# Performance work log

Hardware: AMD Instinct MI355X
Metric: run time of the kernel (lower is better)

Reference implementation:

```python
import jax, jax.numpy as jnp
import numpy as np

B, T = 256, 512          # sequences, timesteps (batched over pyro.markov loop)
DATA_DIM = 88            # piano-roll tones
HIDDEN_DIM = 16          # HMM latent states
NN_DIM = 48
NN_CHANNELS = 2
KERNEL = 3


def _uniform(key, shape, fan_in):
    bound = 1.0 / np.sqrt(fan_in)
    return jax.random.uniform(key, shape, minval=-bound, maxval=bound, dtype=jnp.float32)


def setup_inputs() -> dict:
    key = jax.random.key(0)
    ks = jax.random.split(key, 13)
    w = jax.random.randint(ks[0], (B, T, 1), 0, HIDDEN_DIM)
    x = jax.random.randint(ks[1], (B, T, 1), 0, HIDDEN_DIM)
    y = jax.random.uniform(ks[2], (B, T, DATA_DIM), dtype=jnp.float32)
    return {
        "w": w, "x": x, "y": y,
        # nn.Linear(hidden_dim, nn_dim) for x and w one-hots
        "W_xh": _uniform(ks[3], (NN_DIM, HIDDEN_DIM), HIDDEN_DIM),
        "b_xh": _uniform(ks[4], (NN_DIM,), HIDDEN_DIM),
        "W_wh": _uniform(ks[5], (NN_DIM, HIDDEN_DIM), HIDDEN_DIM),
        "b_wh": _uniform(ks[6], (NN_DIM,), HIDDEN_DIM),
        # nn.Linear(nn_channels*data_dim, nn_dim)
        "W_yh": _uniform(ks[7], (NN_DIM, NN_CHANNELS * DATA_DIM), NN_CHANNELS * DATA_DIM),
        "b_yh": _uniform(ks[8], (NN_DIM,), NN_CHANNELS * DATA_DIM),
        # nn.Conv1d(1, nn_channels, 3, padding=1)
        "W_conv": _uniform(ks[9], (NN_CHANNELS, 1, KERNEL), KERNEL),
        "b_conv": _uniform(ks[10], (NN_CHANNELS,), KERNEL),
        # nn.Linear(nn_dim, data_dim)
        "W_hl": _uniform(ks[11], (DATA_DIM, NN_DIM), NN_DIM),
        "b_hl": _uniform(ks[12], (DATA_DIM,), NN_DIM),
    }


def _tones_generator(w, x, y, W_xh, b_xh, W_wh, b_wh, W_yh, b_yh, W_conv, b_conv, W_hl, b_hl):
    b, t, d = y.shape
    # one-hot scatter of the latent state indices (trailing index dim of size 1)
    w_onehot = jax.nn.one_hot(w[..., 0], HIDDEN_DIM, dtype=y.dtype)   # [B,T,H]
    x_onehot = jax.nn.one_hot(x[..., 0], HIDDEN_DIM, dtype=y.dtype)   # [B,T,H]
    # Conv1d(1 -> nn_channels, k=3, pad=1) over the tone axis
    y_nch = y.reshape(b * t, 1, d)                                    # [BT,1,D]
    y_conv = jax.lax.conv_general_dilated(
        y_nch, W_conv, window_strides=(1,), padding=[(1, 1)],
        dimension_numbers=("NCH", "OIH", "NCH"))
    y_conv = jax.nn.relu(y_conv + b_conv[None, :, None])              # [BT,C,D]
    y_conv = y_conv.reshape(b, t, NN_CHANNELS * d)                    # [B,T,C*D]
    h = jax.nn.relu(
        jnp.einsum("bth,nh->btn", x_onehot, W_xh) + b_xh
        + jnp.einsum("bth,nh->btn", w_onehot, W_wh) + b_wh
        + jnp.einsum("btc,nc->btn", y_conv, W_yh) + b_yh)             # [B,T,ND]
    return jnp.einsum("btn,dn->btd", h, W_hl) + b_hl                  # [B,T,D]


def reference(w, x, y, W_xh, b_xh, W_wh, b_wh, W_yh, b_yh, W_conv, b_conv, W_hl, b_hl):
    return _tones_generator(w, x, y, W_xh, b_xh, W_wh, b_wh, W_yh, b_yh,
                            W_conv, b_conv, W_hl, b_hl)
```

## Files before the change

### kernel.cpp

```cpp
#include <hip/hip_runtime.h>
#include <stdint.h>

#define NTOK (256 * 512)
#define TPB 256

typedef short bf16x8 __attribute__((ext_vector_type(8)));
typedef float f32x4 __attribute__((ext_vector_type(4)));
typedef unsigned short u16;
typedef unsigned int u32;

#define B1_U16 10752
#define B2_U16 6144

__device__ __forceinline__ u16 f2bf(float f) {
    u32 u = __float_as_uint(f);
    return (u16)((u + 0x7fffu + ((u >> 16) & 1u)) >> 16);
}

__global__ __launch_bounds__(256, 1)
void prep_weights(const float* __restrict__ Wxh, const float* __restrict__ bxh,
                  const float* __restrict__ Wwh, const float* __restrict__ bwh,
                  const float* __restrict__ Wyh, const float* __restrict__ byh,
                  const float* __restrict__ Whl, const float* __restrict__ bhl,
                  u16* __restrict__ ws)
{
    int e = blockIdx.x * 256 + threadIdx.x;
    if (e < B1_U16) {
        int j = e & 7, n = (e >> 3) % 48, kc = e / 384;
        int k = kc * 8 + j;
        float v;
        if (k < 176)       v = Wyh[n * 176 + (k & 1) * 88 + (k >> 1)];
        else if (k < 192)  v = Wxh[n * 16 + (k - 176)];
        else if (k < 208)  v = Wwh[n * 16 + (k - 192)];
        else if (k == 208) v = bxh[n] + bwh[n] + byh[n];
        else               v = 0.0f;
        ws[e] = f2bf(v);
    } else if (e < B1_U16 + B2_U16) {
        int e2 = e - B1_U16;
        int j = e2 & 7, dd = (e2 >> 3) % 96, kc = e2 / 768;
        int k = kc * 8 + j;
        float v = 0.0f;
        if (dd < 88) {
            if (k < 48)       v = Whl[dd * 48 + k];
            else if (k == 48) v = bhl[dd];
        }
        ws[e] = f2bf(v);
    }
}

__global__ __launch_bounds__(256, 2)
void tones_v5(const int* __restrict__ widx, const int* __restrict__ xidx,
              const float* __restrict__ y,
              const float* __restrict__ Wconv, const float* __restrict__ bconv,
              const u16* __restrict__ wsb,
              float* __restrict__ out)
{
    __shared__ __align__(16) u16 sH[4 * 1024];

    const int tid = threadIdx.x;
    const int wave = tid >> 6, lane = tid & 63;
    const int q = lane >> 4, c = lane & 15;

    bf16x8 B1[7][3];
    #pragma unroll
    for (int ks = 0; ks < 7; ks++)
        #pragma unroll
        for (int nt = 0; nt < 3; nt++)
            B1[ks][nt] = *(const bf16x8*)(wsb + ((ks * 4 + q) * 48 + nt * 16 + c) * 8);
    bf16x8 B2[2][6];
    #pragma unroll
    for (int ks = 0; ks < 2; ks++)
        #pragma unroll
        for (int nt = 0; nt < 6; nt++)
            B2[ks][nt] = *(const bf16x8*)(wsb + B1_U16 + ((ks * 4 + q) * 96 + nt * 16 + c) * 8);

    const float wc00 = Wconv[0], wc01 = Wconv[1], wc02 = Wconv[2];
    const float wc10 = Wconv[3], wc11 = Wconv[4], wc12 = Wconv[5];
    const float bc0 = bconv[0], bc1 = bconv[1];

    u16* sW = sH + wave * 1024;

    #pragma unroll 1
    for (int t = 0; t < 4; t++) {
        const int tb = blockIdx.x * 256 + wave * 64 + t * 16;
        const float* yc = y + (size_t)(tb + c) * 88;
        const int xv = xidx[tb + c];
        const int wv = widx[tb + c];

        f32x4 h0 = {0, 0, 0, 0}, h1 = {0, 0, 0, 0}, h2 = {0, 0, 0, 0};

        #pragma unroll
        for (int s = 0; s < 5; s++) {
            const int d0 = 16 * s + 4 * q;
            float p0 = (d0 == 0) ? 0.0f : yc[d0 - 1];
            float4 v4 = *(const float4*)(yc + d0);
            float p5 = yc[d0 + 4];
            float p[6] = {p0, v4.x, v4.y, v4.z, v4.w, p5};
            bf16x8 af;
            #pragma unroll
            for (int i = 0; i < 4; i++) {
                float c0 = fmaf(wc00, p[i], fmaf(wc01, p[i + 1], fmaf(wc02, p[i + 2], bc0)));
                float c1 = fmaf(wc10, p[i], fmaf(wc11, p[i + 1], fmaf(wc12, p[i + 2], bc1)));
                af[2 * i]     = (short)f2bf(fmaxf(c0, 0.0f));
                af[2 * i + 1] = (short)f2bf(fmaxf(c1, 0.0f));
            }
            h0 = __builtin_amdgcn_mfma_f32_16x16x32_bf16(af, B1[s][0], h0, 0, 0, 0);
            h1 = __builtin_amdgcn_mfma_f32_16x16x32_bf16(af, B1[s][1], h1, 0, 0, 0);
            h2 = __builtin_amdgcn_mfma_f32_16x16x32_bf16(af, B1[s][2], h2, 0, 0, 0);
        }
        {
            bf16x8 af;
            if (q < 2) {
                const int d0 = 80 + 4 * q;
                float p0 = yc[d0 - 1];
                float4 v4 = *(const float4*)(yc + d0);
                float p5 = (q == 0) ? yc[84] : 0.0f;
                float p[6] = {p0, v4.x, v4.y, v4.z, v4.w, p5};
                #pragma unroll
                for (int i = 0; i < 4; i++) {
                    float c0 = fmaf(wc00, p[i], fmaf(wc01, p[i + 1], fmaf(wc02, p[i + 2], bc0)));
                    float c1 = fmaf(wc10, p[i], fmaf(wc11, p[i + 1], fmaf(wc12, p[i + 2], bc1)));
                    af[2 * i]     = (short)f2bf(fmaxf(c0, 0.0f));
                    af[2 * i + 1] = (short)f2bf(fmaxf(c1, 0.0f));
                }
            } else {
                const int base = (q - 2) * 8;
                #pragma unroll
                for (int j = 0; j < 8; j++)
                    af[j] = (short)((base + j == xv) ? 0x3F80 : 0);
            }
            h0 = __builtin_amdgcn_mfma_f32_16x16x32_bf16(af, B1[5][0], h0, 0, 0, 0);
            h1 = __builtin_amdgcn_mfma_f32_16x16x32_bf16(af, B1[5][1], h1, 0, 0, 0);
            h2 = __builtin_amdgcn_mfma_f32_16x16x32_bf16(af, B1[5][2], h2, 0, 0, 0);
        }
        {
            bf16x8 af;
            if (q < 2) {
                const int base = q * 8;
                #pragma unroll
                for (int j = 0; j < 8; j++)
                    af[j] = (short)((base + j == wv) ? 0x3F80 : 0);
            } else {
                #pragma unroll
                for (int j = 0; j < 8; j++)
                    af[j] = (short)((q == 2 && j == 0) ? 0x3F80 : 0);
            }
            h0 = __builtin_amdgcn_mfma_f32_16x16x32_bf16(af, B1[6][0], h0, 0, 0, 0);
            h1 = __builtin_amdgcn_mfma_f32_16x16x32_bf16(af, B1[6][1], h1, 0, 0, 0);
            h2 = __builtin_amdgcn_mfma_f32_16x16x32_bf16(af, B1[6][2], h2, 0, 0, 0);
        }

        if (lane < 32) {
            uint4 hz = make_uint4((lane < 16) ? 0x3F80u : 0u, 0, 0, 0);
            *(uint4*)(sW + ((6 + (lane >> 4)) * 16 + (lane & 15)) * 8) = hz;
        }
        #pragma unroll
        for (int r = 0; r < 4; r++) {
            const int row = q * 4 + r;
            sW[((0 + (c >> 3)) * 16 + row) * 8 + (c & 7)] = f2bf(fmaxf(h0[r], 0.0f));
            sW[((2 + (c >> 3)) * 16 + row) * 8 + (c & 7)] = f2bf(fmaxf(h1[r], 0.0f));
            sW[((4 + (c >> 3)) * 16 + row) * 8 + (c & 7)] = f2bf(fmaxf(h2[r], 0.0f));
        }

        f32x4 o0 = {0,0,0,0}, o1 = {0,0,0,0}, o2 = {0,0,0,0};
        f32x4 o3 = {0,0,0,0}, o4 = {0,0,0,0}, o5 = {0,0,0,0};
        #pragma unroll
        for (int ks = 0; ks < 2; ks++) {
            bf16x8 a2 = *(const bf16x8*)(sW + ((ks * 4 + q) * 16 + c) * 8);
            o0 = __builtin_amdgcn_mfma_f32_16x16x32_bf16(a2, B2[ks][0], o0, 0, 0, 0);
            o1 = __builtin_amdgcn_mfma_f32_16x16x32_bf16(a2, B2[ks][1], o1, 0, 0, 0);
            o2 = __builtin_amdgcn_mfma_f32_16x16x32_bf16(a2, B2[ks][2], o2, 0, 0, 0);
            o3 = __builtin_amdgcn_mfma_f32_16x16x32_bf16(a2, B2[ks][3], o3, 0, 0, 0);
            o4 = __builtin_amdgcn_mfma_f32_16x16x32_bf16(a2, B2[ks][4], o4, 0, 0, 0);
            o5 = __builtin_amdgcn_mfma_f32_16x16x32_bf16(a2, B2[ks][5], o5, 0, 0, 0);
        }

        float* orow = out + (size_t)(tb + q * 4) * 88;
        #pragma unroll
        for (int r = 0; r < 4; r++) {
            orow[r * 88 +  0 + c] = o0[r];
            orow[r * 88 + 16 + c] = o1[r];
            orow[r * 88 + 32 + c] = o2[r];
            orow[r * 88 + 48 + c] = o3[r];
            orow[r * 88 + 64 + c] = o4[r];
            if (c < 8) orow[r * 88 + 80 + c] = o5[r];
        }
    }
}

extern "C" void kernel_launch(void* const* d_in, const int* in_sizes, int n_in,
                              void* d_out, int out_size, void* d_ws, size_t ws_size,
                              hipStream_t stream) {
    (void)in_sizes; (void)n_in; (void)out_size; (void)ws_size;
    u16* ws = (u16*)d_ws;
    prep_weights<<<dim3(66), dim3(TPB), 0, stream>>>(
        (const float*)d_in[3],  (const float*)d_in[4],
        (const float*)d_in[5],  (const float*)d_in[6],
        (const float*)d_in[7],  (const float*)d_in[8],
        (const float*)d_in[11], (const float*)d_in[12], ws);
    tones_v5<<<dim3(NTOK / 256), dim3(TPB), 0, stream>>>(
        (const int*)d_in[0], (const int*)d_in[1], (const float*)d_in[2],
        (const float*)d_in[9], (const float*)d_in[10], ws, (float*)d_out);
}
```

Measured before the change: 135.6 us.

## Double-buffer y tile loads and stage second-layer weights in LDS

Moves the second-layer weight fragments from registers into shared memory, loaded once per block, which frees registers. Unrolls the four token-tile loop into a software pipeline that prefetches the next tile's y vectors and state indices into registers while the current tile computes. Also hoists the constant bias/zero row write in LDS out of the loop. This adds LDS reads per MFMA and a block barrier, in exchange for more load/compute overlap and lower register pressure.

```diff
diff --git a/kernel.cpp b/kernel.cpp
--- a/kernel.cpp
+++ b/kernel.cpp
@@ -48,54 +48,72 @@
     }
 }
 
+struct Tile { float4 v[6]; int xv, wv; };
+
 __global__ __launch_bounds__(256, 2)
-void tones_v5(const int* __restrict__ widx, const int* __restrict__ xidx,
+void tones_v6(const int* __restrict__ widx, const int* __restrict__ xidx,
               const float* __restrict__ y,
               const float* __restrict__ Wconv, const float* __restrict__ bconv,
               const u16* __restrict__ wsb,
               float* __restrict__ out)
 {
+    __shared__ __align__(16) u16 sB2[B2_U16];
     __shared__ __align__(16) u16 sH[4 * 1024];
 
     const int tid = threadIdx.x;
     const int wave = tid >> 6, lane = tid & 63;
     const int q = lane >> 4, c = lane & 15;
 
+    {
+        const uint4* src = (const uint4*)(wsb + B1_U16);
+        uint4* dst = (uint4*)sB2;
+        #pragma unroll
+        for (int i = 0; i < 3; i++) dst[tid + 256 * i] = src[tid + 256 * i];
+    }
+
     bf16x8 B1[7][3];
     #pragma unroll
     for (int ks = 0; ks < 7; ks++)
         #pragma unroll
         for (int nt = 0; nt < 3; nt++)
             B1[ks][nt] = *(const bf16x8*)(wsb + ((ks * 4 + q) * 48 + nt * 16 + c) * 8);
-    bf16x8 B2[2][6];
-    #pragma unroll
-    for (int ks = 0; ks < 2; ks++)
-        #pragma unroll
-        for (int nt = 0; nt < 6; nt++)
-            B2[ks][nt] = *(const bf16x8*)(wsb + B1_U16 + ((ks * 4 + q) * 96 + nt * 16 + c) * 8);
 
     const float wc00 = Wconv[0], wc01 = Wconv[1], wc02 = Wconv[2];
     const float wc10 = Wconv[3], wc11 = Wconv[4], wc12 = Wconv[5];
     const float bc0 = bconv[0], bc1 = bconv[1];
+    __syncthreads();
 
     u16* sW = sH + wave * 1024;
-
-    #pragma unroll 1
-    for (int t = 0; t < 4; t++) {
-        const int tb = blockIdx.x * 256 + wave * 64 + t * 16;
+    if (lane < 32) {
+        uint4 hz = make_uint4((lane < 16) ? 0x3F80u : 0u, 0, 0, 0);
+        *(uint4*)(sW + ((6 + (lane >> 4)) * 16 + (lane & 15)) * 8) = hz;
+    }
+
+    const int base = blockIdx.x * 256 + wave * 64;
+
+    auto load_tile = [&](int t, Tile& T) {
+        const int tb = base + t * 16;
         const float* yc = y + (size_t)(tb + c) * 88;
-        const int xv = xidx[tb + c];
-        const int wv = widx[tb + c];
-
+        #pragma unroll
+        for (int s = 0; s < 5; s++)
+            T.v[s] = *(const float4*)(yc + 16 * s + 4 * q);
+        if (q < 2) T.v[5] = *(const float4*)(yc + 80 + 4 * q);
+        else       T.v[5] = make_float4(0.f, 0.f, 0.f, 0.f);
+        T.xv = xidx[tb + c];
+        T.wv = widx[tb + c];
+    };
+
+    auto compute_tile = [&](int t, const Tile& T) {
+        const int tb = base + t * 16;
+        const float* yc = y + (size_t)(tb + c) * 88;
         f32x4 h0 = {0, 0, 0, 0}, h1 = {0, 0, 0, 0}, h2 = {0, 0, 0, 0};
 
         #pragma unroll
         for (int s = 0; s < 5; s++) {
             const int d0 = 16 * s + 4 * q;
             float p0 = (d0 == 0) ? 0.0f : yc[d0 - 1];
-            float4 v4 = *(const float4*)(yc + d0);
             float p5 = yc[d0 + 4];
-            float p[6] = {p0, v4.x, v4.y, v4.z, v4.w, p5};
+            float p[6] = {p0, T.v[s].x, T.v[s].y, T.v[s].z, T.v[s].w, p5};
             bf16x8 af;
             #pragma unroll
             for (int i = 0; i < 4; i++) {
@@ -113,9 +131,8 @@
             if (q < 2) {
                 const int d0 = 80 + 4 * q;
                 float p0 = yc[d0 - 1];
-                float4 v4 = *(const float4*)(yc + d0);
                 float p5 = (q == 0) ? yc[84] : 0.0f;
-                float p[6] = {p0, v4.x, v4.y, v4.z, v4.w, p5};
+                float p[6] = {p0, T.v[5].x, T.v[5].y, T.v[5].z, T.v[5].w, p5};
                 #pragma unroll
                 for (int i = 0; i < 4; i++) {
                     float c0 = fmaf(wc00, p[i], fmaf(wc01, p[i + 1], fmaf(wc02, p[i + 2], bc0)));
@@ -124,10 +141,10 @@
                     af[2 * i + 1] = (short)f2bf(fmaxf(c1, 0.0f));
                 }
             } else {
-                const int base = (q - 2) * 8;
+                const int bse = (q - 2) * 8;
                 #pragma unroll
                 for (int j = 0; j < 8; j++)
-                    af[j] = (short)((base + j == xv) ? 0x3F80 : 0);
+                    af[j] = (short)((bse + j == T.xv) ? 0x3F80 : 0);
             }
             h0 = __builtin_amdgcn_mfma_f32_16x16x32_bf16(af, B1[5][0], h0, 0, 0, 0);
             h1 = __builtin_amdgcn_mfma_f32_16x16x32_bf16(af, B1[5][1], h1, 0, 0, 0);
@@ -136,10 +153,10 @@
         {
             bf16x8 af;
             if (q < 2) {
-                const int base = q * 8;
+                const int bse = q * 8;
                 #pragma unroll
                 for (int j = 0; j < 8; j++)
-                    af[j] = (short)((base + j == wv) ? 0x3F80 : 0);
+                    af[j] = (short)((bse + j == T.wv) ? 0x3F80 : 0);
             } else {
                 #pragma unroll
                 for (int j = 0; j < 8; j++)
@@ -150,10 +167,6 @@
             h2 = __builtin_amdgcn_mfma_f32_16x16x32_bf16(af, B1[6][2], h2, 0, 0, 0);
         }
 
-        if (lane < 32) {
-            uint4 hz = make_uint4((lane < 16) ? 0x3F80u : 0u, 0, 0, 0);
-            *(uint4*)(sW + ((6 + (lane >> 4)) * 16 + (lane & 15)) * 8) = hz;
-        }
         #pragma unroll
         for (int r = 0; r < 4; r++) {
             const int row = q * 4 + r;
@@ -167,12 +180,19 @@
         #pragma unroll
         for (int ks = 0; ks < 2; ks++) {
             bf16x8 a2 = *(const bf16x8*)(sW + ((ks * 4 + q) * 16 + c) * 8);
-            o0 = __builtin_amdgcn_mfma_f32_16x16x32_bf16(a2, B2[ks][0], o0, 0, 0, 0);
-            o1 = __builtin_amdgcn_mfma_f32_16x16x32_bf16(a2, B2[ks][1], o1, 0, 0, 0);
-            o2 = __builtin_amdgcn_mfma_f32_16x16x32_bf16(a2, B2[ks][2], o2, 0, 0, 0);
-            o3 = __builtin_amdgcn_mfma_f32_16x16x32_bf16(a2, B2[ks][3], o3, 0, 0, 0);
-            o4 = __builtin_amdgcn_mfma_f32_16x16x32_bf16(a2, B2[ks][4], o4, 0, 0, 0);
-            o5 = __builtin_amdgcn_mfma_f32_16x16x32_bf16(a2, B2[ks][5], o5, 0, 0, 0);
+            bf16x8 b;
+            b = *(const bf16x8*)(sB2 + ((ks * 4 + q) * 96 +  0 + c) * 8);
+            o0 = __builtin_amdgcn_mfma_f32_16x16x32_bf16(a2, b, o0, 0, 0, 0);
+            b = *(const bf16x8*)(sB2 + ((ks * 4 + q) * 96 + 16 + c) * 8);
+            o1 = __builtin_amdgcn_mfma_f32_16x16x32_bf16(a2, b, o1, 0, 0, 0);
+            b = *(const bf16x8*)(sB2 + ((ks * 4 + q) * 96 + 32 + c) * 8);
+            o2 = __builtin_amdgcn_mfma_f32_16x16x32_bf16(a2, b, o2, 0, 0, 0);
+            b = *(const bf16x8*)(sB2 + ((ks * 4 + q) * 96 + 48 + c) * 8);
+            o3 = __builtin_amdgcn_mfma_f32_16x16x32_bf16(a2, b, o3, 0, 0, 0);
+            b = *(const bf16x8*)(sB2 + ((ks * 4 + q) * 96 + 64 + c) * 8);
+            o4 = __builtin_amdgcn_mfma_f32_16x16x32_bf16(a2, b, o4, 0, 0, 0);
+            b = *(const bf16x8*)(sB2 + ((ks * 4 + q) * 96 + 80 + c) * 8);
+            o5 = __builtin_amdgcn_mfma_f32_16x16x32_bf16(a2, b, o5, 0, 0, 0);
         }
 
         float* orow = out + (size_t)(tb + q * 4) * 88;
@@ -185,7 +205,14 @@
             orow[r * 88 + 64 + c] = o4[r];
             if (c < 8) orow[r * 88 + 80 + c] = o5[r];
         }
-    }
+    };
+
+    Tile TA, TB;
+    load_tile(0, TA);
+    load_tile(1, TB);  compute_tile(0, TA);
+    load_tile(2, TA);  compute_tile(1, TB);
+    load_tile(3, TB);  compute_tile(2, TA);
+    compute_tile(3, TB);
 }
 
 extern "C" void kernel_launch(void* const* d_in, const int* in_sizes, int n_in,
@@ -198,7 +225,7 @@
         (const float*)d_in[5],  (const float*)d_in[6],
         (const float*)d_in[7],  (const float*)d_in[8],
         (const float*)d_in[11], (const float*)d_in[12], ws);
-    tones_v5<<<dim3(NTOK / 256), dim3(TPB), 0, stream>>>(
+    tones_v6<<<dim3(NTOK / 256), dim3(TPB), 0, stream>>>(
         (const int*)d_in[0], (const int*)d_in[1], (const float*)d_in[2],
         (const float*)d_in[9], (const float*)d_in[10], ws, (float*)d_out);
 }
```

Measured after the change: 137.0 us. About the same (+1.0%).
